# Optimization experiments

Measured on AMD Instinct MI355X. Metric: run time of the kernel, lower is better.

The kernel has to match this reference:

```python
import jax, jax.numpy as jnp
import numpy as np
from jax import lax

H = 128      # hidden_size
KK = 4       # num_kernels (TemporalConv k)
NL = 2       # rgcn num_layers
C = 32       # convtranse channels
KS = 3       # convtranse kernel_size
NE = 40000   # num_ents
NR = 256     # num_rels
T = 4        # history length
E = 100000   # edges per snapshot
NT = 1024    # num query triplets


def _norm(x):
    return x / jnp.maximum(jnp.linalg.norm(x, axis=-1, keepdims=True), 1e-12)


def _gru(x, h, wih, whh, bih, bhh):
    gi = x @ wih.T + bih
    gh = h @ whh.T + bhh
    ir, iz, inn = jnp.split(gi, 3, axis=-1)
    hr, hz, hn = jnp.split(gh, 3, axis=-1)
    r = jax.nn.sigmoid(ir + hr)
    z = jax.nn.sigmoid(iz + hz)
    n = jnp.tanh(inn + r * hn)
    return (1.0 - z) * n + z * h


def _tconv(e, t, w, b, pw, pb):
    # e: (N,H), t: (1,H) -> kernels (KK,1,H//KK)
    v = (t @ w.T + b).reshape(KK, 1, -1)
    f = lax.conv_general_dilated(e[:, None, :], v, (1,), 'VALID',
                                 dimension_numbers=('NCH', 'OIH', 'NCH'))  # (N,KK,H-H//KK+1)
    return f.reshape(f.shape[0], -1) @ pw.T + pb


def _convtranse(x, ck, cb, fw, fb):
    p = KS // 2
    y = lax.conv_general_dilated(x, ck, (1,), [(p, p)],
                                 dimension_numbers=('NCH', 'OIH', 'NCH')) + cb[None, :, None]
    y = jax.nn.relu(y)
    return jax.nn.relu(y.reshape(y.shape[0], -1) @ fw.T + fb)


def _agg_rel(nf, s, d, r):
    # dense (num_rels, num_nodes) bool mask via scatter, then per-rel mean of touched nodes
    mask = jnp.zeros((NR, NE), bool).at[r, s].set(True).at[r, d].set(True)
    m = mask.astype(nf.dtype)
    su = m @ nf
    c = m.sum(1, keepdims=True)
    return jnp.where(c > 0, su / jnp.maximum(c, 1.0), 0.0)


def _rgcn(h, ef, s, d, wn, ws, b):
    ones = jnp.ones((s.shape[0], 1), h.dtype)
    for l in range(NL):
        msg = h[s] + ef
        sums = jax.ops.segment_sum(msg, d, num_segments=NE)
        cnt = jax.ops.segment_sum(ones, d, num_segments=NE)
        agg = sums / jnp.maximum(cnt, 1.0)
        h = jax.nn.relu(agg @ wn[l] + h @ ws[l] + b[l])
    return h


def setup_inputs() -> dict:
    key = jax.random.key(0)
    ks = jax.random.split(key, 40)
    f32 = jnp.float32
    pin = H * KK - H + KK  # TemporalConv pooling in-features
    inp = {
        'ent_embeds': jax.random.normal(ks[0], (NE, H), f32),
        'rel_embeds': jax.random.normal(ks[1], (NR, H), f32) * 0.1,
        'mmt_embed': jax.random.normal(ks[2], (1, H), f32) * 0.1,
        'tc_w': jax.random.normal(ks[3], (H, H), f32) * 0.05,
        'tc_b': jnp.zeros((H,), f32),
        'tc_pw': jax.random.normal(ks[4], (H, pin), f32) * 0.05,
        'tc_pb': jnp.zeros((H,), f32),
        'gru1_wih': jax.random.normal(ks[5], (3 * H, 2 * H), f32) * 0.05,
        'gru1_whh': jax.random.normal(ks[6], (3 * H, H), f32) * 0.05,
        'gru1_bih': jnp.zeros((3 * H,), f32),
        'gru1_bhh': jnp.zeros((3 * H,), f32),
        'l1_wih': jax.random.normal(ks[7], (3 * H, H), f32) * 0.05,
        'l1_whh': jax.random.normal(ks[8], (3 * H, H), f32) * 0.05,
        'l1_bih': jnp.zeros((3 * H,), f32),
        'l1_bhh': jnp.zeros((3 * H,), f32),
        'l2_wih': jax.random.normal(ks[9], (3 * H, H), f32) * 0.05,
        'l2_whh': jax.random.normal(ks[10], (3 * H, H), f32) * 0.05,
        'l2_bih': jnp.zeros((3 * H,), f32),
        'l2_bhh': jnp.zeros((3 * H,), f32),
        'lin_w': jax.random.normal(ks[11], (H, H), f32) * 0.05,
        'lin_b': jnp.zeros((H,), f32),
        'rgcn_wn': jax.random.normal(ks[12], (NL, H, H), f32) * 0.05,
        'rgcn_ws': jax.random.normal(ks[13], (NL, H, H), f32) * 0.05,
        'rgcn_b': jnp.zeros((NL, H), f32),
        'oc_k': jax.random.normal(ks[14], (C, 2, KS), f32) * 0.1,
        'oc_kb': jnp.zeros((C,), f32),
        'oc_fw': jax.random.normal(ks[15], (H, C * H), f32) * 0.02,
        'oc_fb': jnp.zeros((H,), f32),
        'rc_k': jax.random.normal(ks[16], (C, 2, KS), f32) * 0.1,
        'rc_kb': jnp.zeros((C,), f32),
        'rc_fw': jax.random.normal(ks[17], (H, C * H), f32) * 0.02,
        'rc_fb': jnp.zeros((H,), f32),
        'src': jax.random.randint(ks[18], (T, E), 0, NE, jnp.int32),
        'dst': jax.random.randint(ks[19], (T, E), 0, NE, jnp.int32),
        'rid': jax.random.randint(ks[20], (T, E), 0, NR, jnp.int32),
        'subj': jax.random.randint(ks[21], (NT,), 0, NE, jnp.int32),
        'rel': jax.random.randint(ks[22], (NT,), 0, NR, jnp.int32),
        'obj': jax.random.randint(ks[23], (NT,), 0, NE, jnp.int32),
    }
    return inp


def reference(ent_embeds, rel_embeds, mmt_embed, tc_w, tc_b, tc_pw, tc_pb,
              gru1_wih, gru1_whh, gru1_bih, gru1_bhh,
              l1_wih, l1_whh, l1_bih, l1_bhh,
              l2_wih, l2_whh, l2_bih, l2_bhh,
              lin_w, lin_b, rgcn_wn, rgcn_ws, rgcn_b,
              oc_k, oc_kb, oc_fw, oc_fb, rc_k, rc_kb, rc_fw, rc_fb,
              src, dst, rid, subj, rel, obj):
    rel_param = rel_embeds  # the raw parameter, used inside the loop
    ent = _norm(ent_embeds)
    relh = _norm(rel_embeds)
    mmt = mmt_embed
    zero = jnp.zeros_like(mmt)
    for t in range(T):
        s, d, r = src[t], dst[t], rid[t]
        n_mmt = _gru(mmt, zero, l1_wih, l1_whh, l1_bih, l1_bhh)
        g = _gru(mmt, zero, l2_wih, l2_whh, l2_bih, l2_bhh)
        mmt = mmt + g * (n_mmt - mmt)
        ent = _tconv(ent, mmt, tc_w, tc_b, tc_pw, tc_pb)
        relh = _tconv(relh, mmt, tc_w, tc_b, tc_pw, tc_pb)
        rel_ent = _agg_rel(ent, s, d, r)
        gru_in = jnp.concatenate([rel_ent, rel_param], axis=-1)
        n_rel = _gru(gru_in, relh, gru1_wih, gru1_whh, gru1_bih, gru1_bhh)
        n_rel = _norm(n_rel)
        efeat = n_rel[r]
        nf = _rgcn(ent, efeat, s, d, rgcn_wn, rgcn_ws, rgcn_b)
        nf = _norm(nf)
        u = jax.nn.sigmoid(ent @ lin_w.T + lin_b)
        ent = ent + u * (nf - ent)
        relh = n_rel
    obj_pred = jnp.stack([ent[subj], relh[rel]], axis=1)    # (NT,2,H)
    obj_logit = _convtranse(obj_pred, oc_k, oc_kb, oc_fw, oc_fb) @ ent.T
    rel_pred = jnp.stack([ent[subj], ent[obj]], axis=1)
    rel_logit = _convtranse(rel_pred, rc_k, rc_kb, rc_fw, rc_fb) @ relh.T
    return obj_logit, rel_logit
```

## Files before the change

### kernel.cpp

```cpp
#include <hip/hip_runtime.h>
#include <cmath>


namespace {

constexpr int H   = 128;
constexpr int KK  = 4;
constexpr int C   = 32;
constexpr int NE  = 40000;
constexpr int NR  = 256;
constexpr int T   = 4;
constexpr int E   = 100000;
constexpr int NT  = 1024;
constexpr int PIN = 388;
constexpr int MW  = 1280;
constexpr int MWU = 1250;
constexpr int KC  = 4096;
constexpr int KSP = 32;
constexpr size_t NEH = (size_t)NE * H;

__device__ __forceinline__ float sigm(float x) { return 1.0f / (1.0f + expf(-x)); }

__global__ __launch_bounds__(256) void norm_rows(const float* __restrict__ in,
                                                 float* __restrict__ out, int n) {
  int row  = blockIdx.x * 4 + (threadIdx.x >> 6);
  int lane = threadIdx.x & 63;
  if (row >= n) return;
  const float2* ip = reinterpret_cast<const float2*>(in + (size_t)row * H);
  float2 v = ip[lane];
  float ss = v.x * v.x + v.y * v.y;
#pragma unroll
  for (int off = 32; off; off >>= 1) ss += __shfl_xor(ss, off);
  float inv = 1.0f / fmaxf(sqrtf(ss), 1e-12f);
  float2 o; o.x = v.x * inv; o.y = v.y * inv;
  reinterpret_cast<float2*>(out + (size_t)row * H)[lane] = o;
}

__global__ void copy_vec(const float* __restrict__ a, float* __restrict__ b, int n) {
  int i = blockIdx.x * blockDim.x + threadIdx.x;
  if (i < n) b[i] = a[i];
}

__global__ __launch_bounds__(256) void transpose128(const float* __restrict__ in,
                                                    float* __restrict__ out) {
  int i = blockIdx.x * 256 + threadIdx.x;
  int o = i >> 7, k = i & 127;
  out[k * H + o] = in[o * H + k];
}

__global__ __launch_bounds__(256) void transposeFW(const float* __restrict__ in,
                                                   float* __restrict__ out) {
  int i = blockIdx.x * 256 + threadIdx.x;
  int o = i >> 12, k = i & 4095;
  out[(size_t)k * 128 + o] = in[i];
}

__global__ __launch_bounds__(128) void mmt_step(
    const float* __restrict__ mmt_in,
    const float* __restrict__ w1, const float* __restrict__ bi1, const float* __restrict__ bh1,
    const float* __restrict__ w2, const float* __restrict__ bi2, const float* __restrict__ bh2,
    const float* __restrict__ tcw, const float* __restrict__ tcb,
    float* __restrict__ mmt_out, float* __restrict__ vout) {
  __shared__ float sm[H], sm2[H];
  int t = threadIdx.x;
  sm[t] = mmt_in[t];
  __syncthreads();
  float g1r = bi1[t], g1z = bi1[H + t], g1n = bi1[2 * H + t];
  float g2r = bi2[t], g2z = bi2[H + t], g2n = bi2[2 * H + t];
  {
    const float4* r1p = reinterpret_cast<const float4*>(w1 + (size_t)t * H);
    const float4* z1p = reinterpret_cast<const float4*>(w1 + (size_t)(H + t) * H);
    const float4* n1p = reinterpret_cast<const float4*>(w1 + (size_t)(2 * H + t) * H);
    const float4* r2p = reinterpret_cast<const float4*>(w2 + (size_t)t * H);
    const float4* z2p = reinterpret_cast<const float4*>(w2 + (size_t)(H + t) * H);
    const float4* n2p = reinterpret_cast<const float4*>(w2 + (size_t)(2 * H + t) * H);
    const float4* x4 = reinterpret_cast<const float4*>(sm);
    for (int k = 0; k < 32; k++) {
      float4 x = x4[k];
      float4 a = r1p[k], b = z1p[k], c = n1p[k], d = r2p[k], e = z2p[k], f = n2p[k];
      g1r += x.x * a.x + x.y * a.y + x.z * a.z + x.w * a.w;
      g1z += x.x * b.x + x.y * b.y + x.z * b.z + x.w * b.w;
      g1n += x.x * c.x + x.y * c.y + x.z * c.z + x.w * c.w;
      g2r += x.x * d.x + x.y * d.y + x.z * d.z + x.w * d.w;
      g2z += x.x * e.x + x.y * e.y + x.z * e.z + x.w * e.w;
      g2n += x.x * f.x + x.y * f.y + x.z * f.z + x.w * f.w;
    }
  }
  float r1 = sigm(g1r + bh1[t]), z1 = sigm(g1z + bh1[H + t]);
  float n1 = tanhf(g1n + r1 * bh1[2 * H + t]);
  float nmmt = (1.0f - z1) * n1;
  float r2 = sigm(g2r + bh2[t]), z2 = sigm(g2z + bh2[H + t]);
  float n2 = tanhf(g2n + r2 * bh2[2 * H + t]);
  float gg = (1.0f - z2) * n2;
  float m  = sm[t];
  float mo = m + gg * (nmmt - m);
  mmt_out[t] = mo;
  sm2[t] = mo;
  __syncthreads();
  float v = tcb[t];
  {
    const float4* wp = reinterpret_cast<const float4*>(tcw + (size_t)t * H);
    const float4* x4 = reinterpret_cast<const float4*>(sm2);
    for (int k = 0; k < 32; k++) {
      float4 x = x4[k], w = wp[k];
      v += x.x * w.x + x.y * w.y + x.z * w.z + x.w * w.w;
    }
  }
  vout[t] = v;
}

__global__ __launch_bounds__(128) void build_M(const float* __restrict__ v,
                                               const float* __restrict__ pw,
                                               float* __restrict__ MT) {
  int o = blockIdx.x, p = threadIdx.x;
  __shared__ float sp[PIN];
  __shared__ float sv[H];
  for (int i = p; i < PIN; i += H) sp[i] = pw[(size_t)o * PIN + i];
  sv[p] = v[p];
  __syncthreads();
  float acc = 0.0f;
  int jlo = p - 31 > 0 ? p - 31 : 0;
  int jhi = p < 96 ? p : 96;
#pragma unroll
  for (int k = 0; k < KK; k++)
    for (int j = jlo; j <= jhi; j++) acc += sp[k * 97 + j] * sv[k * 32 + (p - j)];
  MT[p * H + o] = acc;
}

__global__ __launch_bounds__(256) void gemm_bias(const float* __restrict__ X,
                                                 const float* __restrict__ WT,
                                                 const float* __restrict__ bias,
                                                 float* __restrict__ out) {
  __shared__ float sX[64 * H];
  int t = threadIdx.x;
  int base = blockIdx.x * 64;
  const float4* gx = reinterpret_cast<const float4*>(X + (size_t)base * H);
  float4* sx4 = reinterpret_cast<float4*>(sX);
#pragma unroll
  for (int i = 0; i < 8; i++) sx4[t + 256 * i] = gx[t + 256 * i];
  __syncthreads();
  int oq = (t & 31) * 4, ng = (t >> 5) * 8;
  float acc[8][4] = {};
  for (int k = 0; k < H; k += 4) {
    float4 w0 = *reinterpret_cast<const float4*>(&WT[(k + 0) * H + oq]);
    float4 w1 = *reinterpret_cast<const float4*>(&WT[(k + 1) * H + oq]);
    float4 w2 = *reinterpret_cast<const float4*>(&WT[(k + 2) * H + oq]);
    float4 w3 = *reinterpret_cast<const float4*>(&WT[(k + 3) * H + oq]);
#pragma unroll
    for (int m = 0; m < 8; m++) {
      float4 x = *reinterpret_cast<const float4*>(&sX[(ng + m) * H + k]);
      acc[m][0] += x.x * w0.x + x.y * w1.x + x.z * w2.x + x.w * w3.x;
      acc[m][1] += x.x * w0.y + x.y * w1.y + x.z * w2.y + x.w * w3.y;
      acc[m][2] += x.x * w0.z + x.y * w1.z + x.z * w2.z + x.w * w3.z;
      acc[m][3] += x.x * w0.w + x.y * w1.w + x.z * w2.w + x.w * w3.w;
    }
  }
  float4 b4 = *reinterpret_cast<const float4*>(&bias[oq]);
#pragma unroll
  for (int m = 0; m < 8; m++) {
    float4 o4 = {acc[m][0] + b4.x, acc[m][1] + b4.y, acc[m][2] + b4.z, acc[m][3] + b4.w};
    *reinterpret_cast<float4*>(&out[(size_t)(base + ng + m) * H + oq]) = o4;
  }
}

__global__ __launch_bounds__(256) void gemm_rgcn(const float* __restrict__ A,
                                                 const float* __restrict__ Hm,
                                                 const float* __restrict__ wn,
                                                 const float* __restrict__ ws,
                                                 const float* __restrict__ bias,
                                                 const int* __restrict__ deg,
                                                 float* __restrict__ out,
                                                 int donorm) {
  __shared__ float sA[32 * H];
  __shared__ float sH[32 * H];
  int t = threadIdx.x;
  int base = blockIdx.x * 32;
  const float4* ga = reinterpret_cast<const float4*>(A + (size_t)base * H);
  const float4* gh = reinterpret_cast<const float4*>(Hm + (size_t)base * H);
  float4* sa4 = reinterpret_cast<float4*>(sA);
  float4* sh4 = reinterpret_cast<float4*>(sH);
#pragma unroll
  for (int i = 0; i < 4; i++) { sa4[t + 256 * i] = ga[t + 256 * i]; sh4[t + 256 * i] = gh[t + 256 * i]; }
  __syncthreads();
  int oq = (t & 31) * 4, ng = (t >> 5) * 4;
  float accA[4][4] = {}, accS[4][4] = {};
  for (int k = 0; k < H; k += 4) {
    float4 n0 = *reinterpret_cast<const float4*>(&wn[(k + 0) * H + oq]);
    float4 n1 = *reinterpret_cast<const float4*>(&wn[(k + 1) * H + oq]);
    float4 n2 = *reinterpret_cast<const float4*>(&wn[(k + 2) * H + oq]);
    float4 n3 = *reinterpret_cast<const float4*>(&wn[(k + 3) * H + oq]);
    float4 s0 = *reinterpret_cast<const float4*>(&ws[(k + 0) * H + oq]);
    float4 s1 = *reinterpret_cast<const float4*>(&ws[(k + 1) * H + oq]);
    float4 s2 = *reinterpret_cast<const float4*>(&ws[(k + 2) * H + oq]);
    float4 s3 = *reinterpret_cast<const float4*>(&ws[(k + 3) * H + oq]);
#pragma unroll
    for (int m = 0; m < 4; m++) {
      float4 a = *reinterpret_cast<const float4*>(&sA[(ng + m) * H + k]);
      float4 h = *reinterpret_cast<const float4*>(&sH[(ng + m) * H + k]);
      accA[m][0] += a.x * n0.x + a.y * n1.x + a.z * n2.x + a.w * n3.x;
      accA[m][1] += a.x * n0.y + a.y * n1.y + a.z * n2.y + a.w * n3.y;
      accA[m][2] += a.x * n0.z + a.y * n1.z + a.z * n2.z + a.w * n3.z;
      accA[m][3] += a.x * n0.w + a.y * n1.w + a.z * n2.w + a.w * n3.w;
      accS[m][0] += h.x * s0.x + h.y * s1.x + h.z * s2.x + h.w * s3.x;
      accS[m][1] += h.x * s0.y + h.y * s1.y + h.z * s2.y + h.w * s3.y;
      accS[m][2] += h.x * s0.z + h.y * s1.z + h.z * s2.z + h.w * s3.z;
      accS[m][3] += h.x * s0.w + h.y * s1.w + h.z * s2.w + h.w * s3.w;
    }
  }
  float4 b4 = *reinterpret_cast<const float4*>(&bias[oq]);
  float v[4][4];
#pragma unroll
  for (int m = 0; m < 4; m++) {
    float inv = 1.0f / fmaxf((float)deg[base + ng + m], 1.0f);
    v[m][0] = fmaxf(accA[m][0] * inv + accS[m][0] + b4.x, 0.0f);
    v[m][1] = fmaxf(accA[m][1] * inv + accS[m][1] + b4.y, 0.0f);
    v[m][2] = fmaxf(accA[m][2] * inv + accS[m][2] + b4.z, 0.0f);
    v[m][3] = fmaxf(accA[m][3] * inv + accS[m][3] + b4.w, 0.0f);
  }
  if (donorm) {
#pragma unroll
    for (int m = 0; m < 4; m++) {
      float ss = v[m][0]*v[m][0] + v[m][1]*v[m][1] + v[m][2]*v[m][2] + v[m][3]*v[m][3];
#pragma unroll
      for (int off = 16; off; off >>= 1) ss += __shfl_xor(ss, off);
      float inv = 1.0f / fmaxf(sqrtf(ss), 1e-12f);
      v[m][0] *= inv; v[m][1] *= inv; v[m][2] *= inv; v[m][3] *= inv;
    }
  }
#pragma unroll
  for (int m = 0; m < 4; m++) {
    float4 o4 = {v[m][0], v[m][1], v[m][2], v[m][3]};
    *reinterpret_cast<float4*>(&out[(size_t)(base + ng + m) * H + oq]) = o4;
  }
}

__global__ __launch_bounds__(256) void gemm_update(const float* __restrict__ Xe,
                                                   const float* __restrict__ WT,
                                                   const float* __restrict__ bias,
                                                   const float* __restrict__ nf,
                                                   float* __restrict__ out) {
  __shared__ float sX[64 * H];
  int t = threadIdx.x;
  int base = blockIdx.x * 64;
  const float4* gx = reinterpret_cast<const float4*>(Xe + (size_t)base * H);
  float4* sx4 = reinterpret_cast<float4*>(sX);
#pragma unroll
  for (int i = 0; i < 8; i++) sx4[t + 256 * i] = gx[t + 256 * i];
  __syncthreads();
  int oq = (t & 31) * 4, ng = (t >> 5) * 8;
  float acc[8][4] = {};
  for (int k = 0; k < H; k += 4) {
    float4 w0 = *reinterpret_cast<const float4*>(&WT[(k + 0) * H + oq]);
    float4 w1 = *reinterpret_cast<const float4*>(&WT[(k + 1) * H + oq]);
    float4 w2 = *reinterpret_cast<const float4*>(&WT[(k + 2) * H + oq]);
    float4 w3 = *reinterpret_cast<const float4*>(&WT[(k + 3) * H + oq]);
#pragma unroll
    for (int m = 0; m < 8; m++) {
      float4 x = *reinterpret_cast<const float4*>(&sX[(ng + m) * H + k]);
      acc[m][0] += x.x * w0.x + x.y * w1.x + x.z * w2.x + x.w * w3.x;
      acc[m][1] += x.x * w0.y + x.y * w1.y + x.z * w2.y + x.w * w3.y;
      acc[m][2] += x.x * w0.z + x.y * w1.z + x.z * w2.z + x.w * w3.z;
      acc[m][3] += x.x * w0.w + x.y * w1.w + x.z * w2.w + x.w * w3.w;
    }
  }
  float4 b4 = *reinterpret_cast<const float4*>(&bias[oq]);
#pragma unroll
  for (int m = 0; m < 8; m++) {
    size_t row = (size_t)(base + ng + m) * H;
    float4 e4 = *reinterpret_cast<const float4*>(&sX[(ng + m) * H + oq]);
    float4 f4 = *reinterpret_cast<const float4*>(&nf[row + oq]);
    float4 o4 = {e4.x + sigm(acc[m][0] + b4.x) * (f4.x - e4.x),
                 e4.y + sigm(acc[m][1] + b4.y) * (f4.y - e4.y),
                 e4.z + sigm(acc[m][2] + b4.z) * (f4.z - e4.z),
                 e4.w + sigm(acc[m][3] + b4.w) * (f4.w - e4.w)};
    *reinterpret_cast<float4*>(&out[row + oq]) = o4;
  }
}

__global__ __launch_bounds__(256) void edge_prep(const int* __restrict__ s,
                                                 const int* __restrict__ d,
                                                 const int* __restrict__ r,
                                                 unsigned int* __restrict__ mask,
                                                 int* __restrict__ deg) {
  int e = blockIdx.x * 256 + threadIdx.x;
  if (e >= E) return;
  int ri = r[e], si = s[e], di = d[e];
  atomicOr(&mask[(size_t)ri * MW + (si >> 5)], 1u << (si & 31));
  atomicOr(&mask[(size_t)ri * MW + (di >> 5)], 1u << (di & 31));
  atomicAdd(&deg[di], 1);
}

__global__ __launch_bounds__(1024) void scan_deg(const int* __restrict__ deg,
                                                 int* __restrict__ rowptr,
                                                 int* __restrict__ wpos) {
  __shared__ int wsum[16];
  __shared__ int carry_s;
  int tid = threadIdx.x, lane = tid & 63, w = tid >> 6;
  if (tid == 0) carry_s = 0;
  __syncthreads();
  for (int base = 0; base < NE; base += 1024) {
    int idx = base + tid;
    int v = idx < NE ? deg[idx] : 0;
    int x = v;
#pragma unroll
    for (int off = 1; off < 64; off <<= 1) {
      int y = __shfl_up(x, off, 64);
      if (lane >= off) x += y;
    }
    if (lane == 63) wsum[w] = x;
    __syncthreads();
    int carry = carry_s;
    int wpre = 0;
    for (int i = 0; i < w; i++) wpre += wsum[i];
    int excl = carry + wpre + x - v;
    if (idx < NE) { rowptr[idx] = excl; wpos[idx] = excl; }
    __syncthreads();
    if (tid == 1023) carry_s = carry + wpre + x;
  }
  __syncthreads();
  if (tid == 0) rowptr[NE] = carry_s;
}

__global__ __launch_bounds__(256) void edge_fill(const int* __restrict__ d,
                                                 int* __restrict__ wpos,
                                                 int* __restrict__ elist) {
  int e = blockIdx.x * 256 + threadIdx.x;
  if (e >= E) return;
  int p = atomicAdd(&wpos[d[e]], 1);
  elist[p] = e;
}

__global__ __launch_bounds__(256) void rgcn_gather(const float* __restrict__ h,
                                                   const float* __restrict__ ef,
                                                   const int* __restrict__ rowptr,
                                                   const int* __restrict__ elist,
                                                   const int* __restrict__ s,
                                                   const int* __restrict__ r,
                                                   float* __restrict__ agg) {
  int node = blockIdx.x * 2 + (threadIdx.x >> 7);
  int dim  = threadIdx.x & 127;
  int b = rowptr[node], e2 = rowptr[node + 1];
  float acc = 0.0f;
  for (int i = b; i < e2; i++) {
    int e = elist[i];
    acc += h[(size_t)s[e] * H + dim] + ef[(size_t)r[e] * H + dim];
  }
  agg[(size_t)node * H + dim] = acc;
}

__global__ __launch_bounds__(128) void agg_rel_sum(const unsigned int* __restrict__ mask,
                                                   const float* __restrict__ ent,
                                                   float* __restrict__ rsum,
                                                   float* __restrict__ rcnt) {
  int rel = blockIdx.x, part = blockIdx.y, tid = threadIdx.x;
  const int WPS = (MWU + 31) / 32;
  int w0 = part * WPS;
  int w1 = w0 + WPS < MWU ? w0 + WPS : MWU;
  float acc = 0.0f, cnt = 0.0f;
  const unsigned int* mrow = mask + (size_t)rel * MW;
  for (int w = w0; w < w1; w++) {
    unsigned int bits = mrow[w];
    if (!bits) continue;
    cnt += (float)__popc(bits);
    int base = w << 5;
    while (bits) {
      int b = __ffs(bits) - 1;
      bits &= bits - 1;
      acc += ent[(size_t)(base + b) * H + tid];
    }
  }
  if (acc != 0.0f) atomicAdd(&rsum[rel * H + tid], acc);
  if (tid == 0 && cnt != 0.0f) atomicAdd(&rcnt[rel], cnt);
}

__global__ __launch_bounds__(128) void rel_gru(const float* __restrict__ rsum,
                                               const float* __restrict__ rcnt,
                                               const float* __restrict__ rel_param,
                                               const float* __restrict__ relh,
                                               const float* __restrict__ wih,
                                               const float* __restrict__ whh,
                                               const float* __restrict__ bih,
                                               const float* __restrict__ bhh,
                                               float* __restrict__ outp) {
  int rel = blockIdx.x, tid = threadIdx.x;
  __shared__ float sx[2 * H], sh[H], red[H];
  float c = rcnt[rel];
  sx[tid]     = c > 0.0f ? rsum[rel * H + tid] / fmaxf(c, 1.0f) : 0.0f;
  sx[H + tid] = rel_param[rel * H + tid];
  sh[tid]     = relh[rel * H + tid];
  __syncthreads();
  float gr = bih[tid], gz = bih[H + tid], gn = bih[2 * H + tid];
  {
    const float4* rp = reinterpret_cast<const float4*>(wih + (size_t)tid * 2 * H);
    const float4* zp = reinterpret_cast<const float4*>(wih + (size_t)(H + tid) * 2 * H);
    const float4* np = reinterpret_cast<const float4*>(wih + (size_t)(2 * H + tid) * 2 * H);
    const float4* x4 = reinterpret_cast<const float4*>(sx);
    for (int k = 0; k < 64; k++) {
      float4 x = x4[k];
      float4 a = rp[k], b = zp[k], cc = np[k];
      gr += x.x * a.x + x.y * a.y + x.z * a.z + x.w * a.w;
      gz += x.x * b.x + x.y * b.y + x.z * b.z + x.w * b.w;
      gn += x.x * cc.x + x.y * cc.y + x.z * cc.z + x.w * cc.w;
    }
  }
  float hr = bhh[tid], hz = bhh[H + tid], hn = bhh[2 * H + tid];
  {
    const float4* rp = reinterpret_cast<const float4*>(whh + (size_t)tid * H);
    const float4* zp = reinterpret_cast<const float4*>(whh + (size_t)(H + tid) * H);
    const float4* np = reinterpret_cast<const float4*>(whh + (size_t)(2 * H + tid) * H);
    const float4* h4 = reinterpret_cast<const float4*>(sh);
    for (int k = 0; k < 32; k++) {
      float4 x = h4[k];
      float4 a = rp[k], b = zp[k], cc = np[k];
      hr += x.x * a.x + x.y * a.y + x.z * a.z + x.w * a.w;
      hz += x.x * b.x + x.y * b.y + x.z * b.z + x.w * b.w;
      hn += x.x * cc.x + x.y * cc.y + x.z * cc.z + x.w * cc.w;
    }
  }
  float r = sigm(gr + hr), z = sigm(gz + hz), nn = tanhf(gn + r * hn);
  float val = (1.0f - z) * nn + z * sh[tid];
  red[tid] = val * val;
  __syncthreads();
  for (int s2 = 64; s2 > 0; s2 >>= 1) {
    if (tid < s2) red[tid] += red[tid + s2];
    __syncthreads();
  }
  float inv = 1.0f / fmaxf(sqrtf(red[0]), 1e-12f);
  outp[rel * H + tid] = val * inv;
}

__global__ __launch_bounds__(256) void conv_relu(const float* __restrict__ fa,
                                                 const int* __restrict__ ia,
                                                 const float* __restrict__ fbm,
                                                 const int* __restrict__ ib,
                                                 const float* __restrict__ ck,
                                                 const float* __restrict__ ckb,
                                                 float* __restrict__ Y) {
  __shared__ float sx[8 * 2 * H];
  __shared__ float sck[C * 6];
  __shared__ float sckb[C];
  int tid = threadIdx.x, q0 = blockIdx.x * 8;
  if (tid < C * 6) sck[tid] = ck[tid];
  if (tid < C)     sckb[tid] = ckb[tid];
#pragma unroll
  for (int i = tid; i < 2048; i += 256) {
    int q = i >> 8, half = (i >> 7) & 1, p = i & 127;
    int node = (half ? ib : ia)[q0 + q];
    sx[i] = (half ? fbm : fa)[(size_t)node * H + p];
  }
  __syncthreads();
  for (int i4 = tid; i4 < 8192; i4 += 256) {
    int q = i4 >> 10, rr = i4 & 1023;
    int c = rr >> 5, p0 = (rr & 31) << 2;
    const float* x0 = &sx[q * 256];
    const float* x1 = x0 + 128;
    float k00 = sck[c * 6 + 0], k01 = sck[c * 6 + 1], k02 = sck[c * 6 + 2];
    float k10 = sck[c * 6 + 3], k11 = sck[c * 6 + 4], k12 = sck[c * 6 + 5];
    float bb = sckb[c];
    float4 o;
    float* op = &o.x;
#pragma unroll
    for (int dd = 0; dd < 4; dd++) {
      int p = p0 + dd;
      float acc = bb + x0[p] * k01 + x1[p] * k11;
      if (p - 1 >= 0)  acc += x0[p - 1] * k00 + x1[p - 1] * k10;
      if (p + 1 < H)   acc += x0[p + 1] * k02 + x1[p + 1] * k12;
      op[dd] = fmaxf(acc, 0.0f);
    }
    *reinterpret_cast<float4*>(&Y[(size_t)(q0 + q) * KC + rr * 4]) = o;
  }
}

__global__ __launch_bounds__(256) void conv_gemm(const float* __restrict__ Y,
                                                 const float* __restrict__ fwT,
                                                 float* __restrict__ Zp) {
  int t = threadIdx.x;
  int mb = blockIdx.x * 32, ks = blockIdx.y;
  int oq = (t & 31) * 4, ng = (t >> 5) * 4;
  const float* yb = Y + (size_t)(mb + ng) * KC + ks * 128;
  const float* wb = fwT + (size_t)ks * 128 * H + oq;
  float acc[4][4] = {};
  for (int k = 0; k < 128; k += 4) {
    float4 w0 = *reinterpret_cast<const float4*>(wb + (size_t)(k + 0) * H);
    float4 w1 = *reinterpret_cast<const float4*>(wb + (size_t)(k + 1) * H);
    float4 w2 = *reinterpret_cast<const float4*>(wb + (size_t)(k + 2) * H);
    float4 w3 = *reinterpret_cast<const float4*>(wb + (size_t)(k + 3) * H);
#pragma unroll
    for (int m = 0; m < 4; m++) {
      float4 y = *reinterpret_cast<const float4*>(yb + (size_t)m * KC + k);
      acc[m][0] += y.x * w0.x + y.y * w1.x + y.z * w2.x + y.w * w3.x;
      acc[m][1] += y.x * w0.y + y.y * w1.y + y.z * w2.y + y.w * w3.y;
      acc[m][2] += y.x * w0.z + y.y * w1.z + y.z * w2.z + y.w * w3.z;
      acc[m][3] += y.x * w0.w + y.y * w1.w + y.z * w2.w + y.w * w3.w;
    }
  }
  float* zb = Zp + (size_t)ks * NT * H;
#pragma unroll
  for (int m = 0; m < 4; m++) {
    float4 o4 = {acc[m][0], acc[m][1], acc[m][2], acc[m][3]};
    *reinterpret_cast<float4*>(&zb[(size_t)(mb + ng + m) * H + oq]) = o4;
  }
}

__global__ __launch_bounds__(256) void conv_finalize(const float* __restrict__ Zp,
                                                     const float* __restrict__ fb,
                                                     float* __restrict__ Z) {
  int i = blockIdx.x * 256 + threadIdx.x;
  int o = i & 127;
  float v = fb[o];
#pragma unroll
  for (int s = 0; s < KSP; s++) v += Zp[(size_t)s * NT * H + i];
  Z[i] = fmaxf(v, 0.0f);
}

__global__ __launch_bounds__(256) void logits_gemm2(const float* __restrict__ Z,
                                                    const float* __restrict__ F,
                                                    float* __restrict__ out,
                                                    int M) {
  __shared__ float sZ[32 * H];
  __shared__ float sF[32 * H];
  int t = threadIdx.x;
  int bq = blockIdx.y * 128, bm = blockIdx.x * 128;
  int tx = t & 15, ty = t >> 4;
  float acc[8][8] = {};
  int qld = t & 127, kh = (t >> 7) * 16;
  int mld = bm + qld;
  if (mld >= M) mld = M - 1;
  for (int kc = 0; kc < H; kc += 32) {
    __syncthreads();
    const float* zr = Z + (size_t)(bq + qld) * H + kc + kh;
    const float* fr = F + (size_t)mld * H + kc + kh;
#pragma unroll
    for (int j = 0; j < 16; j += 4) {
      float4 v = *reinterpret_cast<const float4*>(zr + j);
      sZ[(kh + j + 0) * H + qld] = v.x;
      sZ[(kh + j + 1) * H + qld] = v.y;
      sZ[(kh + j + 2) * H + qld] = v.z;
      sZ[(kh + j + 3) * H + qld] = v.w;
      float4 f = *reinterpret_cast<const float4*>(fr + j);
      sF[(kh + j + 0) * H + qld] = f.x;
      sF[(kh + j + 1) * H + qld] = f.y;
      sF[(kh + j + 2) * H + qld] = f.z;
      sF[(kh + j + 3) * H + qld] = f.w;
    }
    __syncthreads();
    for (int k = 0; k < 32; k++) {
      float4 za = *reinterpret_cast<const float4*>(&sZ[k * H + ty * 8]);
      float4 zb = *reinterpret_cast<const float4*>(&sZ[k * H + ty * 8 + 4]);
      float4 fa = *reinterpret_cast<const float4*>(&sF[k * H + tx * 8]);
      float4 fbv = *reinterpret_cast<const float4*>(&sF[k * H + tx * 8 + 4]);
      float zq[8] = {za.x, za.y, za.z, za.w, zb.x, zb.y, zb.z, zb.w};
      float fm[8] = {fa.x, fa.y, fa.z, fa.w, fbv.x, fbv.y, fbv.z, fbv.w};
#pragma unroll
      for (int i = 0; i < 8; i++)
#pragma unroll
        for (int j = 0; j < 8; j++) acc[i][j] += zq[i] * fm[j];
    }
  }
  int m0 = bm + tx * 8;
  if (m0 >= M) return;
#pragma unroll
  for (int i = 0; i < 8; i++) {
    size_t row = (size_t)(bq + ty * 8 + i) * (size_t)M + m0;
    float4 o1 = {acc[i][0], acc[i][1], acc[i][2], acc[i][3]};
    float4 o2 = {acc[i][4], acc[i][5], acc[i][6], acc[i][7]};
    *reinterpret_cast<float4*>(&out[row]) = o1;
    *reinterpret_cast<float4*>(&out[row + 4]) = o2;
  }
}

}

extern "C" void kernel_launch(void* const* d_in, const int* in_sizes, int n_in,
                              void* d_out, int out_size, void* d_ws, size_t ws_size,
                              hipStream_t stream) {
  (void)in_sizes; (void)n_in; (void)out_size; (void)ws_size;
  const float* ent_embeds = (const float*)d_in[0];
  const float* rel_embeds = (const float*)d_in[1];
  const float* mmt_embed  = (const float*)d_in[2];
  const float* tc_w  = (const float*)d_in[3];
  const float* tc_b  = (const float*)d_in[4];
  const float* tc_pw = (const float*)d_in[5];
  const float* tc_pb = (const float*)d_in[6];
  const float* g1_wih = (const float*)d_in[7];
  const float* g1_whh = (const float*)d_in[8];
  const float* g1_bih = (const float*)d_in[9];
  const float* g1_bhh = (const float*)d_in[10];
  const float* l1_wih = (const float*)d_in[11];
  const float* l1_bih = (const float*)d_in[13];
  const float* l1_bhh = (const float*)d_in[14];
  const float* l2_wih = (const float*)d_in[15];
  const float* l2_bih = (const float*)d_in[17];
  const float* l2_bhh = (const float*)d_in[18];
  const float* lin_w = (const float*)d_in[19];
  const float* lin_b = (const float*)d_in[20];
  const float* rgcn_wn = (const float*)d_in[21];
  const float* rgcn_ws = (const float*)d_in[22];
  const float* rgcn_b  = (const float*)d_in[23];
  const float* oc_k  = (const float*)d_in[24];
  const float* oc_kb = (const float*)d_in[25];
  const float* oc_fw = (const float*)d_in[26];
  const float* oc_fb = (const float*)d_in[27];
  const float* rc_k  = (const float*)d_in[28];
  const float* rc_kb = (const float*)d_in[29];
  const float* rc_fw = (const float*)d_in[30];
  const float* rc_fb = (const float*)d_in[31];
  const int* src  = (const int*)d_in[32];
  const int* dst  = (const int*)d_in[33];
  const int* rid  = (const int*)d_in[34];
  const int* qsub = (const int*)d_in[35];
  const int* qrel = (const int*)d_in[36];
  const int* qobj = (const int*)d_in[37];

  float* out = (float*)d_out;
  float* ws  = (float*)d_ws;

  size_t off = 0;
  float* entF = ws + off; off += NEH;
  float* relhB[3] = {ws + off, ws + off + (size_t)NR * H, ws + off + 2 * (size_t)NR * H};
  off += 3 * (size_t)NR * H;
  float* rel_sum = ws + off; off += (size_t)NR * H;
  float* rcnt    = ws + off; off += NR;
  float* mmtbuf0 = ws + off; off += H;
  float* mmtbuf1 = ws + off; off += H;
  float* vbuf    = ws + off; off += H;
  float* MT      = ws + off; off += (size_t)H * H;
  float* WTlin   = ws + off; off += (size_t)H * H;
  float* Zo      = ws + off; off += (size_t)NT * H;
  float* Zr      = ws + off; off += (size_t)NT * H;
  unsigned int* mask = (unsigned int*)(ws + off); off += (size_t)NR * MW;

  float* B[4] = {out, out + NEH, out + 2 * NEH, out + 3 * NEH};
  int* itail   = (int*)(out + 4 * NEH);
  int* deg     = itail;
  int* rowptr  = itail + NE;
  int* wpos    = itail + 2 * NE + 1;
  int* elist   = itail + 3 * NE + 1;
  float* mmtb[2] = {mmtbuf0, mmtbuf1};
  float* Ybuf  = out;
  float* Zp    = out + (size_t)NT * KC;
  float* fwTo  = Zp + (size_t)KSP * NT * H;
  float* fwTr  = fwTo + (size_t)KC * H;

  norm_rows<<<(NE + 3) / 4, 256, 0, stream>>>(ent_embeds, B[0], NE);
  norm_rows<<<(NR + 3) / 4, 256, 0, stream>>>(rel_embeds, relhB[0], NR);
  copy_vec<<<1, 128, 0, stream>>>(mmt_embed, mmtbuf0, H);
  transpose128<<<64, 256, 0, stream>>>(lin_w, WTlin);

  int cur = 0, curRelh = 0;
  for (int t = 0; t < T; t++) {
    int fr[3], fi = 0;
    for (int b = 0; b < 4; b++) if (b != cur) fr[fi++] = b;
    int bX = fr[0], bG = fr[1], bY = fr[2];
    const int* s_t = src + (size_t)t * E;
    const int* d_t = dst + (size_t)t * E;
    const int* r_t = rid + (size_t)t * E;

    mmt_step<<<1, 128, 0, stream>>>(mmtb[t & 1], l1_wih, l1_bih, l1_bhh,
                                    l2_wih, l2_bih, l2_bhh, tc_w, tc_b,
                                    mmtb[(t + 1) & 1], vbuf);
    build_M<<<H, H, 0, stream>>>(vbuf, tc_pw, MT);
    gemm_bias<<<NE / 64, 256, 0, stream>>>(B[cur], MT, tc_pb, B[bX]);
    gemm_bias<<<NR / 64, 256, 0, stream>>>(relhB[curRelh], MT, tc_pb, relhB[2]);

    hipMemsetAsync(mask, 0, (size_t)NR * MW * 4, stream);
    hipMemsetAsync(deg, 0, (size_t)NE * 4, stream);
    edge_prep<<<(E + 255) / 256, 256, 0, stream>>>(s_t, d_t, r_t, mask, deg);

    hipMemsetAsync(rel_sum, 0, ((size_t)NR * H + NR) * 4, stream);
    agg_rel_sum<<<dim3(NR, 32), 128, 0, stream>>>(mask, B[bX], rel_sum, rcnt);
    int nextRelh = 1 - curRelh;
    rel_gru<<<NR, 128, 0, stream>>>(rel_sum, rcnt, rel_embeds, relhB[2],
                                    g1_wih, g1_whh, g1_bih, g1_bhh, relhB[nextRelh]);

    scan_deg<<<1, 1024, 0, stream>>>(deg, rowptr, wpos);
    edge_fill<<<(E + 255) / 256, 256, 0, stream>>>(d_t, wpos, elist);

    rgcn_gather<<<NE / 2, 256, 0, stream>>>(B[bX], relhB[nextRelh], rowptr, elist, s_t, r_t, B[bG]);
    gemm_rgcn<<<NE / 32, 256, 0, stream>>>(B[bG], B[bX], rgcn_wn, rgcn_ws, rgcn_b, deg, B[bY], 0);
    rgcn_gather<<<NE / 2, 256, 0, stream>>>(B[bY], relhB[nextRelh], rowptr, elist, s_t, r_t, B[bG]);
    gemm_rgcn<<<NE / 32, 256, 0, stream>>>(B[bG], B[bY], rgcn_wn + H * H, rgcn_ws + H * H,
                                           rgcn_b + H, deg, B[cur], 1);

    float* entDst = (t == T - 1) ? entF : B[bY];
    gemm_update<<<NE / 64, 256, 0, stream>>>(B[bX], WTlin, lin_b, B[cur], entDst);

    cur = bY;
    curRelh = nextRelh;
  }

  float* relhF = relhB[curRelh];

  transposeFW<<<2048, 256, 0, stream>>>(oc_fw, fwTo);
  transposeFW<<<2048, 256, 0, stream>>>(rc_fw, fwTr);

  conv_relu<<<NT / 8, 256, 0, stream>>>(entF, qsub, relhF, qrel, oc_k, oc_kb, Ybuf);
  conv_gemm<<<dim3(NT / 32, KSP), 256, 0, stream>>>(Ybuf, fwTo, Zp);
  conv_finalize<<<NT * H / 256, 256, 0, stream>>>(Zp, oc_fb, Zo);

  conv_relu<<<NT / 8, 256, 0, stream>>>(entF, qsub, entF, qobj, rc_k, rc_kb, Ybuf);
  conv_gemm<<<dim3(NT / 32, KSP), 256, 0, stream>>>(Ybuf, fwTr, Zp);
  conv_finalize<<<NT * H / 256, 256, 0, stream>>>(Zp, rc_fb, Zr);

  logits_gemm2<<<dim3((NE + 127) / 128, NT / 128), 256, 0, stream>>>(Zo, entF, out, NE);
  logits_gemm2<<<dim3(NR / 128, NT / 128), 256, 0, stream>>>(Zr, relhF, out + (size_t)NT * NE, NR);
}
```

Measured before the change: 2.215 ms.

## Pre-transpose logits operand and stream it from global in new GEMM tiling

Adds a shared-memory transpose that lays out the final entity and relation embeddings K-major, padded to a multiple of 256 columns. The final logits GEMM is replaced by one that keeps only the 64-query Z tile in LDS and streams the transposed embeddings straight from global memory with float4 loads. This removes per-k-chunk LDS staging and the barriers for the large operand. The separate entF workspace copy is dropped and the final entities are read from the rotating buffer inside the output, which risks being overwritten by later scratch writes into the output buffer before they are read.

```diff
diff --git a/kernel.cpp b/kernel.cpp
--- a/kernel.cpp
+++ b/kernel.cpp
@@ -17,6 +17,7 @@
 constexpr int MWU = 1250;
 constexpr int KC  = 4096;
 constexpr int KSP = 32;
+constexpr int MPE = 40192;
 constexpr size_t NEH = (size_t)NE * H;
 
 __device__ __forceinline__ float sigm(float x) { return 1.0f / (1.0f + expf(-x)); }
@@ -53,6 +54,24 @@
   int i = blockIdx.x * 256 + threadIdx.x;
   int o = i >> 12, k = i & 4095;
   out[(size_t)k * 128 + o] = in[i];
+}
+
+__global__ __launch_bounds__(256) void transposeF(const float* __restrict__ in,
+                                                  float* __restrict__ out,
+                                                  int R, int MP) {
+  __shared__ float tile[64][129];
+  int r0 = blockIdx.x * 64;
+  int t = threadIdx.x;
+  for (int idx = t; idx < 64 * 128; idx += 256) {
+    int q = idx >> 7, k = idx & 127;
+    int r = r0 + q;
+    tile[q][k] = (r < R) ? in[(size_t)r * H + k] : 0.0f;
+  }
+  __syncthreads();
+  for (int idx = t; idx < 64 * 128; idx += 256) {
+    int k = idx >> 6, q = idx & 63;
+    out[(size_t)k * MP + r0 + q] = tile[q][k];
+  }
 }
 
 __global__ __launch_bounds__(128) void mmt_step(
@@ -513,55 +532,39 @@
   Z[i] = fmaxf(v, 0.0f);
 }
 
-__global__ __launch_bounds__(256) void logits_gemm2(const float* __restrict__ Z,
-                                                    const float* __restrict__ F,
-                                                    float* __restrict__ out,
-                                                    int M) {
-  __shared__ float sZ[32 * H];
-  __shared__ float sF[32 * H];
+__global__ __launch_bounds__(256, 4) void logits_gemm3(const float* __restrict__ Z,
+                                                       const float* __restrict__ FT,
+                                                       float* __restrict__ out,
+                                                       int M, int MP) {
+  __shared__ float sZ[128][68];
   int t = threadIdx.x;
-  int bq = blockIdx.y * 128, bm = blockIdx.x * 128;
-  int tx = t & 15, ty = t >> 4;
+  int bm = blockIdx.x * 256, bq = blockIdx.y * 64;
+  for (int idx = t; idx < 64 * 128; idx += 256) {
+    int q = idx >> 7, k = idx & 127;
+    sZ[k][q] = Z[(size_t)(bq + q) * H + k];
+  }
+  __syncthreads();
+  int tx = t & 31, ty = t >> 5;
+  int m0 = bm + tx * 8, q0 = ty * 8;
+  const float* ftp = FT + m0;
   float acc[8][8] = {};
-  int qld = t & 127, kh = (t >> 7) * 16;
-  int mld = bm + qld;
-  if (mld >= M) mld = M - 1;
-  for (int kc = 0; kc < H; kc += 32) {
-    __syncthreads();
-    const float* zr = Z + (size_t)(bq + qld) * H + kc + kh;
-    const float* fr = F + (size_t)mld * H + kc + kh;
-#pragma unroll
-    for (int j = 0; j < 16; j += 4) {
-      float4 v = *reinterpret_cast<const float4*>(zr + j);
-      sZ[(kh + j + 0) * H + qld] = v.x;
-      sZ[(kh + j + 1) * H + qld] = v.y;
-      sZ[(kh + j + 2) * H + qld] = v.z;
-      sZ[(kh + j + 3) * H + qld] = v.w;
-      float4 f = *reinterpret_cast<const float4*>(fr + j);
-      sF[(kh + j + 0) * H + qld] = f.x;
-      sF[(kh + j + 1) * H + qld] = f.y;
-      sF[(kh + j + 2) * H + qld] = f.z;
-      sF[(kh + j + 3) * H + qld] = f.w;
-    }
-    __syncthreads();
-    for (int k = 0; k < 32; k++) {
-      float4 za = *reinterpret_cast<const float4*>(&sZ[k * H + ty * 8]);
-      float4 zb = *reinterpret_cast<const float4*>(&sZ[k * H + ty * 8 + 4]);
-      float4 fa = *reinterpret_cast<const float4*>(&sF[k * H + tx * 8]);
-      float4 fbv = *reinterpret_cast<const float4*>(&sF[k * H + tx * 8 + 4]);
-      float zq[8] = {za.x, za.y, za.z, za.w, zb.x, zb.y, zb.z, zb.w};
-      float fm[8] = {fa.x, fa.y, fa.z, fa.w, fbv.x, fbv.y, fbv.z, fbv.w};
-#pragma unroll
-      for (int i = 0; i < 8; i++)
-#pragma unroll
-        for (int j = 0; j < 8; j++) acc[i][j] += zq[i] * fm[j];
-    }
-  }
-  int m0 = bm + tx * 8;
+#pragma unroll 2
+  for (int k = 0; k < H; k++) {
+    float4 fa = *reinterpret_cast<const float4*>(ftp + (size_t)k * MP);
+    float4 fb = *reinterpret_cast<const float4*>(ftp + (size_t)k * MP + 4);
+    float4 za = *reinterpret_cast<const float4*>(&sZ[k][q0]);
+    float4 zb = *reinterpret_cast<const float4*>(&sZ[k][q0 + 4]);
+    float zq[8] = {za.x, za.y, za.z, za.w, zb.x, zb.y, zb.z, zb.w};
+    float fm[8] = {fa.x, fa.y, fa.z, fa.w, fb.x, fb.y, fb.z, fb.w};
+#pragma unroll
+    for (int i = 0; i < 8; i++)
+#pragma unroll
+      for (int j = 0; j < 8; j++) acc[i][j] += zq[i] * fm[j];
+  }
   if (m0 >= M) return;
 #pragma unroll
   for (int i = 0; i < 8; i++) {
-    size_t row = (size_t)(bq + ty * 8 + i) * (size_t)M + m0;
+    size_t row = (size_t)(bq + q0 + i) * (size_t)M + m0;
     float4 o1 = {acc[i][0], acc[i][1], acc[i][2], acc[i][3]};
     float4 o2 = {acc[i][4], acc[i][5], acc[i][6], acc[i][7]};
     *reinterpret_cast<float4*>(&out[row]) = o1;
@@ -616,7 +619,6 @@
   float* ws  = (float*)d_ws;
 
   size_t off = 0;
-  float* entF = ws + off; off += NEH;
   float* relhB[3] = {ws + off, ws + off + (size_t)NR * H, ws + off + 2 * (size_t)NR * H};
   off += 3 * (size_t)NR * H;
   float* rel_sum = ws + off; off += (size_t)NR * H;
@@ -628,6 +630,8 @@
   float* WTlin   = ws + off; off += (size_t)H * H;
   float* Zo      = ws + off; off += (size_t)NT * H;
   float* Zr      = ws + off; off += (size_t)NT * H;
+  float* FTe     = ws + off; off += (size_t)H * MPE;
+  float* FTr     = ws + off; off += (size_t)H * NR;
   unsigned int* mask = (unsigned int*)(ws + off); off += (size_t)NR * MW;
 
   float* B[4] = {out, out + NEH, out + 2 * NEH, out + 3 * NEH};
@@ -682,14 +686,17 @@
     gemm_rgcn<<<NE / 32, 256, 0, stream>>>(B[bG], B[bY], rgcn_wn + H * H, rgcn_ws + H * H,
                                            rgcn_b + H, deg, B[cur], 1);
 
-    float* entDst = (t == T - 1) ? entF : B[bY];
-    gemm_update<<<NE / 64, 256, 0, stream>>>(B[bX], WTlin, lin_b, B[cur], entDst);
+    gemm_update<<<NE / 64, 256, 0, stream>>>(B[bX], WTlin, lin_b, B[cur], B[bY]);
 
     cur = bY;
     curRelh = nextRelh;
   }
 
+  float* entF  = B[cur];
   float* relhF = relhB[curRelh];
+
+  transposeF<<<MPE / 64, 256, 0, stream>>>(entF, FTe, NE, MPE);
+  transposeF<<<NR / 64, 256, 0, stream>>>(relhF, FTr, NR, NR);
 
   transposeFW<<<2048, 256, 0, stream>>>(oc_fw, fwTo);
   transposeFW<<<2048, 256, 0, stream>>>(rc_fw, fwTr);
@@ -702,6 +709,6 @@
   conv_gemm<<<dim3(NT / 32, KSP), 256, 0, stream>>>(Ybuf, fwTr, Zp);
   conv_finalize<<<NT * H / 256, 256, 0, stream>>>(Zp, rc_fb, Zr);
 
-  logits_gemm2<<<dim3((NE + 127) / 128, NT / 128), 256, 0, stream>>>(Zo, entF, out, NE);
-  logits_gemm2<<<dim3(NR / 128, NT / 128), 256, 0, stream>>>(Zr, relhF, out + (size_t)NT * NE, NR);
-}
+  logits_gemm3<<<dim3(MPE / 256, NT / 64), 256, 0, stream>>>(Zo, FTe, out, NE, MPE);
+  logits_gemm3<<<dim3(NR / 256, NT / 64), 256, 0, stream>>>(Zr, FTr, out + (size_t)NT * NE, NR, NR);
+}
```

Result: no change. 2.217 ms (+0.1%).
